# Kernel optimization log

Measured on AMD Instinct MI355X. Metric: run time of the kernel, lower is better.

## Reference

```python
import jax, jax.numpy as jnp
import numpy as np

B, L, D = 2, 384, 128
N, DHS, DHP = 8, 16, 4  # heads, scalar head dim, point head dim
D_SCALAR = N * DHS          # 128
D_POINT = N * DHP * 3       # 96
D_OUT_IN = D_SCALAR + D * N + D_POINT + N * DHP  # 1280


def setup_inputs() -> dict:
    key = jax.random.key(0)
    ks = jax.random.split(key, 14)
    sc = 0.05
    x = jax.random.normal(ks[0], (B, L, D), dtype=jnp.float32)
    e = jax.random.normal(ks[1], (B, L, L, D), dtype=jnp.float32)
    r = jax.random.normal(ks[2], (B, L, 3, 3), dtype=jnp.float32)
    t = jax.random.normal(ks[3], (B, L, 3), dtype=jnp.float32)
    Wq_s = jax.random.normal(ks[4], (D, D_SCALAR)) * sc
    Wk_s = jax.random.normal(ks[5], (D, D_SCALAR)) * sc
    Wv_s = jax.random.normal(ks[6], (D, D_SCALAR)) * sc
    Wb = jax.random.normal(ks[7], (D, N)) * sc
    Wq_p = jax.random.normal(ks[8], (D, D_POINT)) * sc
    Wk_p = jax.random.normal(ks[9], (D, D_POINT)) * sc
    Wv_p = jax.random.normal(ks[10], (D, D_POINT)) * sc
    gamma = jnp.full((N,), float(np.log(np.exp(1.0) - 1.0)), dtype=jnp.float32)
    Wo = jax.random.normal(ks[11], (D_OUT_IN, D)) * sc
    bo = jnp.zeros((D,), dtype=jnp.float32)
    return {"x": x, "e": e, "r": r, "t": t, "Wq_s": Wq_s, "Wk_s": Wk_s,
            "Wv_s": Wv_s, "Wb": Wb, "Wq_p": Wq_p, "Wk_p": Wk_p,
            "Wv_p": Wv_p, "gamma": gamma, "Wo": Wo, "bo": bo}


def _heads_scalar(y):  # (b,l,n*d) -> (b,n,l,d)
    b, l, _ = y.shape
    return y.reshape(b, l, N, DHS).transpose(0, 2, 1, 3)


def _heads_point(y):  # (b,l,n*p*3) -> (b,n,l,p,3)
    b, l, _ = y.shape
    return y.reshape(b, l, N, DHP, 3).transpose(0, 2, 1, 3, 4)


def reference(x, e, r, t, Wq_s, Wk_s, Wv_s, Wb, Wq_p, Wk_p, Wv_p, gamma, Wo, bo):
    b, l, _ = x.shape
    qs = _heads_scalar(x @ Wq_s)
    ks_ = _heads_scalar(x @ Wk_s)
    vs = _heads_scalar(x @ Wv_s)

    # local points -> global frame: x_row @ r + t (note row-vector convention)
    t_b = t[:, None, :, None, :]  # (b,1,l,1,3)
    qp = jnp.einsum('bnlpk,blkc->bnlpc', _heads_point(x @ Wq_p), r) + t_b
    kp = jnp.einsum('bnlpk,blkc->bnlpc', _heads_point(x @ Wk_p), r) + t_b
    vp = jnp.einsum('bnlpk,blkc->bnlpc', _heads_point(x @ Wv_p), r) + t_b

    logit_scalar = jnp.einsum('bnid,bnjd->bnij', qs, ks_) * (DHS ** -0.5)
    bias_pair = jnp.einsum('bijd,dn->bnij', e, Wb)

    # sum_{p,c} (q_i - k_j)^2 via norm expansion (same math, no O(l^2 p 3) tensor)
    qq = jnp.sum(qp * qp, axis=(-1, -2))  # (b,n,i)
    kk = jnp.sum(kp * kp, axis=(-1, -2))  # (b,n,j)
    cross = jnp.einsum('bnipc,bnjpc->bnij', qp, kp)
    dist2 = qq[..., :, None] + kk[..., None, :] - 2.0 * cross
    logit_point = (-0.5 * 0.25) * gamma[None, :, None, None] * dist2

    logit = (3.0 ** -0.5) * (logit_scalar + bias_pair + logit_point)
    attn = jax.nn.softmax(logit, axis=-1)  # (b,n,i,j)

    out_scalar = jnp.einsum('bnij,bnjd->bnid', attn, vs)
    out_scalar = out_scalar.transpose(0, 2, 1, 3).reshape(b, l, N * DHS)

    out_pair = jnp.einsum('bnij,bijd->bnid', attn, e)
    out_pair = out_pair.transpose(0, 2, 1, 3).reshape(b, l, N * D)

    op = jnp.einsum('bnij,bnjpc->bnipc', attn, vp)
    # inverse transform: (x - t) @ r^T  -> out[c] = sum_k (x-t)[k] * r[c,k]
    op_local = jnp.einsum('bnipk,bick->bnipc', op - t_b, r)
    op_norm = jnp.linalg.norm(op_local, axis=-1)  # (b,n,i,p)

    out_point = op_local.transpose(0, 2, 1, 3, 4).reshape(b, l, N * DHP * 3)
    out_norm = op_norm.transpose(0, 2, 1, 3).reshape(b, l, N * DHP)

    out = jnp.concatenate([out_scalar, out_pair, out_point, out_norm], axis=-1)
    return out @ Wo + bo
```

## Files before the change

### kernel.cpp

```cpp
#include <hip/hip_runtime.h>
#include <hip/hip_bf16.h>

#define BB 2
#define LL 384
#define DD 128
#define NH 8

typedef const float* fp32p;

__global__ __launch_bounds__(128) void k_proj(
    fp32p x, fp32p r, fp32p tvec,
    fp32p Wqs, fp32p Wks, fp32p Wvs,
    fp32p Wqp, fp32p Wkp, fp32p Wvp,
    float* qs, float* ks, float* vs,
    float* qp, float* kp, float* vp)
{
  int bl = blockIdx.x;
  int t = threadIdx.x;
  __shared__ float xs[128];
  __shared__ float yq[96], yk[96], yv[96];
  xs[t] = x[bl*128 + t];
  __syncthreads();
  float aq = 0.f, ak = 0.f, av = 0.f;
  for (int d = 0; d < 128; ++d) {
    float xv = xs[d];
    aq += xv * Wqs[d*128 + t];
    ak += xv * Wks[d*128 + t];
    av += xv * Wvs[d*128 + t];
  }
  int b = bl / LL, l = bl - (bl / LL) * LL;
  int n = t >> 4, dhs = t & 15;
  int rowbase = (b*NH + n)*LL + l;
  qs[rowbase*16 + dhs] = aq;
  ks[rowbase*16 + dhs] = ak;
  vs[rowbase*16 + dhs] = av;
  if (t < 96) {
    float pq = 0.f, pk = 0.f, pv = 0.f;
    for (int d = 0; d < 128; ++d) {
      float xv = xs[d];
      pq += xv * Wqp[d*96 + t];
      pk += xv * Wkp[d*96 + t];
      pv += xv * Wvp[d*96 + t];
    }
    yq[t] = pq; yk[t] = pk; yv[t] = pv;
  }
  __syncthreads();
  if (t < 96) {
    int np = t / 12;
    int rem = t - np*12;
    int p = rem / 3, c = rem - p*3;
    float rr0 = r[(bl*3 + 0)*3 + c];
    float rr1 = r[(bl*3 + 1)*3 + c];
    float rr2 = r[(bl*3 + 2)*3 + c];
    float tt  = tvec[bl*3 + c];
    int base = np*12 + p*3;
    int prow = (b*NH + np)*LL + l;
    qp[prow*12 + p*3 + c] = yq[base]*rr0 + yq[base+1]*rr1 + yq[base+2]*rr2 + tt;
    kp[prow*12 + p*3 + c] = yk[base]*rr0 + yk[base+1]*rr1 + yk[base+2]*rr2 + tt;
    vp[prow*12 + p*3 + c] = yv[base]*rr0 + yv[base+1]*rr1 + yv[base+2]*rr2 + tt;
  }
}

__global__ __launch_bounds__(256) void k_bias(fp32p e, fp32p Wb, float* bias)
{
  __shared__ float WbS[128*8];
  for (int idx = threadIdx.x; idx < 1024; idx += 256) WbS[idx] = Wb[idx];
  __syncthreads();
  int tid = blockIdx.x*256 + threadIdx.x;
  int b = tid / (LL*LL);
  int rem = tid - b*(LL*LL);
  int i = rem / LL, j = rem - (rem / LL)*LL;
  const float4* erow = reinterpret_cast<const float4*>(e) + (size_t)tid * 32;
  float acc[8] = {0,0,0,0,0,0,0,0};
  for (int it = 0; it < 32; ++it) {
    float4 v4 = erow[it];
    float vv[4] = {v4.x, v4.y, v4.z, v4.w};
    #pragma unroll
    for (int k = 0; k < 4; ++k) {
      float v = vv[k];
      const float* wr = &WbS[(it*4 + k)*8];
      #pragma unroll
      for (int nn = 0; nn < 8; ++nn) acc[nn] += v * wr[nn];
    }
  }
  #pragma unroll
  for (int nn = 0; nn < 8; ++nn)
    bias[(((size_t)(b*NH + nn)*LL + i)*LL) + j] = acc[nn];
}

__global__ __launch_bounds__(256) void k_attn(
    const float* qs, const float* ks, const float* qp, const float* kp,
    fp32p gamma, float* attn)
{
  int row = blockIdx.x*4 + (threadIdx.x >> 6);
  int lane = threadIdx.x & 63;
  int bn = row / LL;
  int n = bn & 7;
  int rowbase = bn * LL;
  float q[16];
  const float4* q4 = reinterpret_cast<const float4*>(qs + (size_t)row*16);
  #pragma unroll
  for (int k2 = 0; k2 < 4; ++k2) { float4 v = q4[k2]; q[4*k2]=v.x; q[4*k2+1]=v.y; q[4*k2+2]=v.z; q[4*k2+3]=v.w; }
  float qpv[12];
  const float4* p4 = reinterpret_cast<const float4*>(qp + (size_t)row*12);
  #pragma unroll
  for (int k2 = 0; k2 < 3; ++k2) { float4 v = p4[k2]; qpv[4*k2]=v.x; qpv[4*k2+1]=v.y; qpv[4*k2+2]=v.z; qpv[4*k2+3]=v.w; }
  float qq = 0.f;
  #pragma unroll
  for (int k2 = 0; k2 < 12; ++k2) qq += qpv[k2]*qpv[k2];
  float coef = -0.125f * gamma[n];
  float lg[6];
  float* arow = attn + (size_t)row*LL;
  #pragma unroll
  for (int jj = 0; jj < 6; ++jj) {
    int j = lane + jj*64;
    const float4* k4 = reinterpret_cast<const float4*>(ks + (size_t)(rowbase + j)*16);
    float dots = 0.f;
    #pragma unroll
    for (int k2 = 0; k2 < 4; ++k2) { float4 v = k4[k2]; dots += q[4*k2]*v.x + q[4*k2+1]*v.y + q[4*k2+2]*v.z + q[4*k2+3]*v.w; }
    const float4* kp4 = reinterpret_cast<const float4*>(kp + (size_t)(rowbase + j)*12);
    float cross = 0.f, kk = 0.f;
    #pragma unroll
    for (int k2 = 0; k2 < 3; ++k2) {
      float4 v = kp4[k2];
      cross += qpv[4*k2]*v.x + qpv[4*k2+1]*v.y + qpv[4*k2+2]*v.z + qpv[4*k2+3]*v.w;
      kk += v.x*v.x + v.y*v.y + v.z*v.z + v.w*v.w;
    }
    float bs = arow[j];
    lg[jj] = 0.57735027f * (0.25f*dots + bs + coef*(qq + kk - 2.f*cross));
  }
  float m = lg[0];
  #pragma unroll
  for (int jj = 1; jj < 6; ++jj) m = fmaxf(m, lg[jj]);
  #pragma unroll
  for (int off = 32; off >= 1; off >>= 1) m = fmaxf(m, __shfl_xor(m, off, 64));
  float el[6]; float s = 0.f;
  #pragma unroll
  for (int jj = 0; jj < 6; ++jj) { el[jj] = __expf(lg[jj] - m); s += el[jj]; }
  #pragma unroll
  for (int off = 32; off >= 1; off >>= 1) s += __shfl_xor(s, off, 64);
  float inv = 1.f / s;
  #pragma unroll
  for (int jj = 0; jj < 6; ++jj) arow[lane + jj*64] = el[jj]*inv;
}

__global__ __launch_bounds__(256) void k_av(
    const float* attn, const float* vs, const float* vp, float* cat, float* opb)
{
  int tid = blockIdx.x*256 + threadIdx.x;
  int row = tid >> 5;
  int dim = tid & 31;
  if (dim >= 28) return;
  int i = row % LL;
  int bn = row / LL;
  int rowbase = bn * LL;
  const float* arow = attn + (size_t)row*LL;
  const float* src; int stride;
  if (dim < 16) { src = vs + (size_t)rowbase*16 + dim; stride = 16; }
  else          { src = vp + (size_t)rowbase*12 + (dim - 16); stride = 12; }
  float acc = 0.f;
  for (int j = 0; j < LL; ++j) acc += arow[j] * src[(size_t)j*stride];
  int b = bn >> 3, n = bn & 7;
  if (dim < 16) cat[((size_t)(b*LL + i))*1280 + n*16 + dim] = acc;
  else          opb[(size_t)row*12 + (dim - 16)] = acc;
}

__global__ __launch_bounds__(256) void k_pair(fp32p e, const float* attn, float* cat)
{
  int bi = blockIdx.x;
  int b = bi / LL, i = bi - (bi / LL)*LL;
  __shared__ float attnS[8*384];
  __shared__ float redS[128*9];
  for (int idx = threadIdx.x; idx < 8*384; idx += 256) {
    int n = idx / 384, j = idx - n*384;
    attnS[idx] = attn[(((size_t)(b*NH + n)*LL + i)*LL) + j];
  }
  __syncthreads();
  int t = threadIdx.x;
  int oct = t & 15;
  int n = (t >> 4) & 7;
  int half = t >> 7;
  const float4* ebase = reinterpret_cast<const float4*>(e) + (size_t)bi*LL*32;
  const float* an = attnS + n*384;
  float acc[8] = {0,0,0,0,0,0,0,0};
  for (int jj = 0; jj < 192; ++jj) {
    int j = 2*jj + half;
    float4 va = ebase[j*32 + oct*2];
    float4 vb = ebase[j*32 + oct*2 + 1];
    float a = an[j];
    acc[0] += a * va.x; acc[1] += a * va.y; acc[2] += a * va.z; acc[3] += a * va.w;
    acc[4] += a * vb.x; acc[5] += a * vb.y; acc[6] += a * vb.z; acc[7] += a * vb.w;
  }
  if (half) {
    #pragma unroll
    for (int k = 0; k < 8; ++k) redS[(t - 128)*9 + k] = acc[k];
  }
  __syncthreads();
  if (!half) {
    float* dst = cat + (size_t)bi*1280 + 128 + n*128 + oct*8;
    #pragma unroll
    for (int k = 0; k < 8; ++k) dst[k] = acc[k] + redS[t*9 + k];
  }
}

__global__ __launch_bounds__(256) void k_pt(const float* opb, fp32p r, fp32p tvec, float* cat)
{
  int tid = blockIdx.x*256 + threadIdx.x;
  int p = tid & 3;
  int row = tid >> 2;
  int i = row % LL;
  int bn = row / LL;
  int b = bn >> 3, n = bn & 7;
  int bi = b*LL + i;
  float o[3];
  #pragma unroll
  for (int k = 0; k < 3; ++k)
    o[k] = opb[(size_t)row*12 + p*3 + k] - tvec[bi*3 + k];
  float loc[3];
  #pragma unroll
  for (int c = 0; c < 3; ++c) {
    float s = 0.f;
    #pragma unroll
    for (int k = 0; k < 3; ++k) s += o[k] * r[(bi*3 + c)*3 + k];
    loc[c] = s;
  }
  float* dst = cat + (size_t)bi*1280;
  dst[1152 + n*12 + p*3 + 0] = loc[0];
  dst[1152 + n*12 + p*3 + 1] = loc[1];
  dst[1152 + n*12 + p*3 + 2] = loc[2];
  dst[1248 + n*4 + p] = sqrtf(loc[0]*loc[0] + loc[1]*loc[1] + loc[2]*loc[2]);
}

__global__ __launch_bounds__(128) void k_out(const float* cat, fp32p Wo, fp32p bo,
                                             float* out)
{
  __shared__ float catS[4*1280];
  int row0 = blockIdx.x*4;
  for (int idx = threadIdx.x; idx < 4*1280; idx += 128)
    catS[idx] = cat[(size_t)row0*1280 + idx];
  __syncthreads();
  int t = threadIdx.x;
  float bov = bo[t];
  float a0 = bov, a1 = bov, a2 = bov, a3 = bov;
  for (int k = 0; k < 1280; ++k) {
    float w = Wo[k*128 + t];
    a0 += catS[k]        * w;
    a1 += catS[1280 + k] * w;
    a2 += catS[2560 + k] * w;
    a3 += catS[3840 + k] * w;
  }
  out[(size_t)(row0 + 0)*128 + t] = a0;
  out[(size_t)(row0 + 1)*128 + t] = a1;
  out[(size_t)(row0 + 2)*128 + t] = a2;
  out[(size_t)(row0 + 3)*128 + t] = a3;
}

extern "C" void kernel_launch(void* const* d_in, const int* in_sizes, int n_in,
                              void* d_out, int out_size, void* d_ws, size_t ws_size,
                              hipStream_t stream)
{
  fp32p x    = (fp32p)d_in[0];
  fp32p e    = (fp32p)d_in[1];
  fp32p r    = (fp32p)d_in[2];
  fp32p tv   = (fp32p)d_in[3];
  fp32p Wqs  = (fp32p)d_in[4];
  fp32p Wks  = (fp32p)d_in[5];
  fp32p Wvs  = (fp32p)d_in[6];
  fp32p Wb   = (fp32p)d_in[7];
  fp32p Wqp  = (fp32p)d_in[8];
  fp32p Wkp  = (fp32p)d_in[9];
  fp32p Wvp  = (fp32p)d_in[10];
  fp32p gam  = (fp32p)d_in[11];
  fp32p Wo   = (fp32p)d_in[12];
  fp32p bo   = (fp32p)d_in[13];
  float* out = (float*)d_out;

  float* qs   = (float*)d_ws;
  float* ks   = qs + 98304;
  float* vs   = ks + 98304;
  float* qp   = vs + 98304;
  float* kp   = qp + 73728;
  float* vp   = kp + 73728;
  float* attn = vp + 73728;
  float* opb  = attn + 2359296;
  float* cat  = opb + 73728;

  k_proj<<<768, 128, 0, stream>>>(x, r, tv, Wqs, Wks, Wvs, Wqp, Wkp, Wvp,
                                  qs, ks, vs, qp, kp, vp);
  k_bias<<<1152, 256, 0, stream>>>(e, Wb, attn);
  k_attn<<<1536, 256, 0, stream>>>(qs, ks, qp, kp, gam, attn);
  k_av<<<768, 256, 0, stream>>>(attn, vs, vp, cat, opb);
  k_pair<<<768, 256, 0, stream>>>(e, attn, cat);
  k_pt<<<96, 256, 0, stream>>>(opb, r, tv, cat);
  k_out<<<192, 128, 0, stream>>>(cat, Wo, bo, out);
}
```

Before: 422.3 us.

## Fuse bias, logits, softmax, AV, pair and point stages into one per-row kernel

```diff
diff --git a/kernel.cpp b/kernel.cpp
--- a/kernel.cpp
+++ b/kernel.cpp
@@ -1,9 +1,6 @@
 #include <hip/hip_runtime.h>
-#include <hip/hip_bf16.h>
-
-#define BB 2
+
 #define LL 384
-#define DD 128
 #define NH 8
 
 typedef const float* fp32p;
@@ -15,244 +12,242 @@
     float* qs, float* ks, float* vs,
     float* qp, float* kp, float* vp)
 {
-  int bl = blockIdx.x;
   int t = threadIdx.x;
-  __shared__ float xs[128];
-  __shared__ float yq[96], yk[96], yv[96];
-  xs[t] = x[bl*128 + t];
-  __syncthreads();
-  float aq = 0.f, ak = 0.f, av = 0.f;
+  int bl0 = blockIdx.x * 4;
+  __shared__ float xs[4][128];
+  __shared__ float yq[4][96], yk[4][96], yv[4][96];
+  #pragma unroll
+  for (int rr = 0; rr < 4; ++rr) xs[rr][t] = x[(bl0 + rr)*128 + t];
+  __syncthreads();
+  float aq[4] = {0,0,0,0}, ak[4] = {0,0,0,0}, av[4] = {0,0,0,0};
+  float pq[4] = {0,0,0,0}, pk[4] = {0,0,0,0}, pv[4] = {0,0,0,0};
+  bool pt_act = (t < 96);
   for (int d = 0; d < 128; ++d) {
-    float xv = xs[d];
-    aq += xv * Wqs[d*128 + t];
-    ak += xv * Wks[d*128 + t];
-    av += xv * Wvs[d*128 + t];
-  }
-  int b = bl / LL, l = bl - (bl / LL) * LL;
+    float wq = Wqs[d*128 + t], wk = Wks[d*128 + t], wv = Wvs[d*128 + t];
+    #pragma unroll
+    for (int rr = 0; rr < 4; ++rr) {
+      float xv = xs[rr][d];
+      aq[rr] += xv*wq; ak[rr] += xv*wk; av[rr] += xv*wv;
+    }
+    if (pt_act) {
+      float uq = Wqp[d*96 + t], uk = Wkp[d*96 + t], uv = Wvp[d*96 + t];
+      #pragma unroll
+      for (int rr = 0; rr < 4; ++rr) {
+        float xv = xs[rr][d];
+        pq[rr] += xv*uq; pk[rr] += xv*uk; pv[rr] += xv*uv;
+      }
+    }
+  }
   int n = t >> 4, dhs = t & 15;
-  int rowbase = (b*NH + n)*LL + l;
-  qs[rowbase*16 + dhs] = aq;
-  ks[rowbase*16 + dhs] = ak;
-  vs[rowbase*16 + dhs] = av;
-  if (t < 96) {
-    float pq = 0.f, pk = 0.f, pv = 0.f;
-    for (int d = 0; d < 128; ++d) {
-      float xv = xs[d];
-      pq += xv * Wqp[d*96 + t];
-      pk += xv * Wkp[d*96 + t];
-      pv += xv * Wvp[d*96 + t];
-    }
-    yq[t] = pq; yk[t] = pk; yv[t] = pv;
-  }
-  __syncthreads();
-  if (t < 96) {
+  #pragma unroll
+  for (int rr = 0; rr < 4; ++rr) {
+    int bl = bl0 + rr;
+    int b = bl / LL, l = bl - (bl / LL)*LL;
+    int rowbase = (b*NH + n)*LL + l;
+    qs[rowbase*16 + dhs] = aq[rr];
+    ks[rowbase*16 + dhs] = ak[rr];
+    vs[rowbase*16 + dhs] = av[rr];
+  }
+  if (pt_act) {
+    #pragma unroll
+    for (int rr = 0; rr < 4; ++rr) { yq[rr][t] = pq[rr]; yk[rr][t] = pk[rr]; yv[rr][t] = pv[rr]; }
+  }
+  __syncthreads();
+  if (pt_act) {
     int np = t / 12;
     int rem = t - np*12;
     int p = rem / 3, c = rem - p*3;
-    float rr0 = r[(bl*3 + 0)*3 + c];
-    float rr1 = r[(bl*3 + 1)*3 + c];
-    float rr2 = r[(bl*3 + 2)*3 + c];
-    float tt  = tvec[bl*3 + c];
     int base = np*12 + p*3;
-    int prow = (b*NH + np)*LL + l;
-    qp[prow*12 + p*3 + c] = yq[base]*rr0 + yq[base+1]*rr1 + yq[base+2]*rr2 + tt;
-    kp[prow*12 + p*3 + c] = yk[base]*rr0 + yk[base+1]*rr1 + yk[base+2]*rr2 + tt;
-    vp[prow*12 + p*3 + c] = yv[base]*rr0 + yv[base+1]*rr1 + yv[base+2]*rr2 + tt;
-  }
-}
-
-__global__ __launch_bounds__(256) void k_bias(fp32p e, fp32p Wb, float* bias)
-{
-  __shared__ float WbS[128*8];
-  for (int idx = threadIdx.x; idx < 1024; idx += 256) WbS[idx] = Wb[idx];
-  __syncthreads();
-  int tid = blockIdx.x*256 + threadIdx.x;
-  int b = tid / (LL*LL);
-  int rem = tid - b*(LL*LL);
-  int i = rem / LL, j = rem - (rem / LL)*LL;
-  const float4* erow = reinterpret_cast<const float4*>(e) + (size_t)tid * 32;
-  float acc[8] = {0,0,0,0,0,0,0,0};
-  for (int it = 0; it < 32; ++it) {
-    float4 v4 = erow[it];
-    float vv[4] = {v4.x, v4.y, v4.z, v4.w};
-    #pragma unroll
-    for (int k = 0; k < 4; ++k) {
-      float v = vv[k];
-      const float* wr = &WbS[(it*4 + k)*8];
-      #pragma unroll
-      for (int nn = 0; nn < 8; ++nn) acc[nn] += v * wr[nn];
-    }
-  }
-  #pragma unroll
-  for (int nn = 0; nn < 8; ++nn)
-    bias[(((size_t)(b*NH + nn)*LL + i)*LL) + j] = acc[nn];
-}
-
-__global__ __launch_bounds__(256) void k_attn(
-    const float* qs, const float* ks, const float* qp, const float* kp,
-    fp32p gamma, float* attn)
-{
-  int row = blockIdx.x*4 + (threadIdx.x >> 6);
-  int lane = threadIdx.x & 63;
-  int bn = row / LL;
-  int n = bn & 7;
-  int rowbase = bn * LL;
-  float q[16];
-  const float4* q4 = reinterpret_cast<const float4*>(qs + (size_t)row*16);
-  #pragma unroll
-  for (int k2 = 0; k2 < 4; ++k2) { float4 v = q4[k2]; q[4*k2]=v.x; q[4*k2+1]=v.y; q[4*k2+2]=v.z; q[4*k2+3]=v.w; }
-  float qpv[12];
-  const float4* p4 = reinterpret_cast<const float4*>(qp + (size_t)row*12);
-  #pragma unroll
-  for (int k2 = 0; k2 < 3; ++k2) { float4 v = p4[k2]; qpv[4*k2]=v.x; qpv[4*k2+1]=v.y; qpv[4*k2+2]=v.z; qpv[4*k2+3]=v.w; }
-  float qq = 0.f;
-  #pragma unroll
-  for (int k2 = 0; k2 < 12; ++k2) qq += qpv[k2]*qpv[k2];
-  float coef = -0.125f * gamma[n];
-  float lg[6];
-  float* arow = attn + (size_t)row*LL;
-  #pragma unroll
-  for (int jj = 0; jj < 6; ++jj) {
-    int j = lane + jj*64;
-    const float4* k4 = reinterpret_cast<const float4*>(ks + (size_t)(rowbase + j)*16);
-    float dots = 0.f;
-    #pragma unroll
-    for (int k2 = 0; k2 < 4; ++k2) { float4 v = k4[k2]; dots += q[4*k2]*v.x + q[4*k2+1]*v.y + q[4*k2+2]*v.z + q[4*k2+3]*v.w; }
-    const float4* kp4 = reinterpret_cast<const float4*>(kp + (size_t)(rowbase + j)*12);
-    float cross = 0.f, kk = 0.f;
-    #pragma unroll
-    for (int k2 = 0; k2 < 3; ++k2) {
-      float4 v = kp4[k2];
-      cross += qpv[4*k2]*v.x + qpv[4*k2+1]*v.y + qpv[4*k2+2]*v.z + qpv[4*k2+3]*v.w;
-      kk += v.x*v.x + v.y*v.y + v.z*v.z + v.w*v.w;
-    }
-    float bs = arow[j];
-    lg[jj] = 0.57735027f * (0.25f*dots + bs + coef*(qq + kk - 2.f*cross));
-  }
-  float m = lg[0];
-  #pragma unroll
-  for (int jj = 1; jj < 6; ++jj) m = fmaxf(m, lg[jj]);
-  #pragma unroll
-  for (int off = 32; off >= 1; off >>= 1) m = fmaxf(m, __shfl_xor(m, off, 64));
-  float el[6]; float s = 0.f;
-  #pragma unroll
-  for (int jj = 0; jj < 6; ++jj) { el[jj] = __expf(lg[jj] - m); s += el[jj]; }
-  #pragma unroll
-  for (int off = 32; off >= 1; off >>= 1) s += __shfl_xor(s, off, 64);
-  float inv = 1.f / s;
-  #pragma unroll
-  for (int jj = 0; jj < 6; ++jj) arow[lane + jj*64] = el[jj]*inv;
-}
-
-__global__ __launch_bounds__(256) void k_av(
-    const float* attn, const float* vs, const float* vp, float* cat, float* opb)
-{
-  int tid = blockIdx.x*256 + threadIdx.x;
-  int row = tid >> 5;
-  int dim = tid & 31;
-  if (dim >= 28) return;
-  int i = row % LL;
-  int bn = row / LL;
-  int rowbase = bn * LL;
-  const float* arow = attn + (size_t)row*LL;
-  const float* src; int stride;
-  if (dim < 16) { src = vs + (size_t)rowbase*16 + dim; stride = 16; }
-  else          { src = vp + (size_t)rowbase*12 + (dim - 16); stride = 12; }
-  float acc = 0.f;
-  for (int j = 0; j < LL; ++j) acc += arow[j] * src[(size_t)j*stride];
-  int b = bn >> 3, n = bn & 7;
-  if (dim < 16) cat[((size_t)(b*LL + i))*1280 + n*16 + dim] = acc;
-  else          opb[(size_t)row*12 + (dim - 16)] = acc;
-}
-
-__global__ __launch_bounds__(256) void k_pair(fp32p e, const float* attn, float* cat)
+    #pragma unroll
+    for (int rr = 0; rr < 4; ++rr) {
+      int bl = bl0 + rr;
+      int b = bl / LL, l = bl - (bl / LL)*LL;
+      float rr0 = r[(bl*3 + 0)*3 + c];
+      float rr1 = r[(bl*3 + 1)*3 + c];
+      float rr2 = r[(bl*3 + 2)*3 + c];
+      float tt  = tvec[bl*3 + c];
+      int prow = (b*NH + np)*LL + l;
+      qp[prow*12 + p*3 + c] = yq[rr][base]*rr0 + yq[rr][base+1]*rr1 + yq[rr][base+2]*rr2 + tt;
+      kp[prow*12 + p*3 + c] = yk[rr][base]*rr0 + yk[rr][base+1]*rr1 + yk[rr][base+2]*rr2 + tt;
+      vp[prow*12 + p*3 + c] = yv[rr][base]*rr0 + yv[rr][base+1]*rr1 + yv[rr][base+2]*rr2 + tt;
+    }
+  }
+}
+
+__global__ __launch_bounds__(256) void k_fused(
+    fp32p e, fp32p Wb, fp32p gamma, fp32p r, fp32p tvec,
+    const float* qs, const float* ks, const float* vs,
+    const float* qp, const float* kp, const float* vp,
+    float* cat)
 {
   int bi = blockIdx.x;
   int b = bi / LL, i = bi - (bi / LL)*LL;
-  __shared__ float attnS[8*384];
+  int t = threadIdx.x;
+  __shared__ float attnS[8*385];
   __shared__ float redS[128*9];
-  for (int idx = threadIdx.x; idx < 8*384; idx += 256) {
-    int n = idx / 384, j = idx - n*384;
-    attnS[idx] = attn[(((size_t)(b*NH + n)*LL + i)*LL) + j];
-  }
-  __syncthreads();
+  __shared__ float opS[96];
+
+  const float* ebase = e + (size_t)bi*LL*128;
+
+  for (int j = t; j < LL; j += 256) {
+    const float4* er = reinterpret_cast<const float4*>(ebase + j*128);
+    float accb[8] = {0,0,0,0,0,0,0,0};
+    for (int it = 0; it < 32; ++it) {
+      float4 v4 = er[it];
+      float vv[4] = {v4.x, v4.y, v4.z, v4.w};
+      #pragma unroll
+      for (int k = 0; k < 4; ++k) {
+        float ev = vv[k];
+        int d = it*4 + k;
+        #pragma unroll
+        for (int nn = 0; nn < 8; ++nn) accb[nn] += ev * Wb[d*8 + nn];
+      }
+    }
+    #pragma unroll
+    for (int nn = 0; nn < 8; ++nn) {
+      int rowq = (b*NH + nn)*LL + i;
+      int rowk = (b*NH + nn)*LL + j;
+      const float4* k4  = reinterpret_cast<const float4*>(ks + (size_t)rowk*16);
+      const float4* q4  = reinterpret_cast<const float4*>(qs + (size_t)rowq*16);
+      float dots = 0.f;
+      #pragma unroll
+      for (int k2 = 0; k2 < 4; ++k2) {
+        float4 kv = k4[k2]; float4 qv = q4[k2];
+        dots += qv.x*kv.x + qv.y*kv.y + qv.z*kv.z + qv.w*kv.w;
+      }
+      const float4* kp4 = reinterpret_cast<const float4*>(kp + (size_t)rowk*12);
+      const float4* qp4 = reinterpret_cast<const float4*>(qp + (size_t)rowq*12);
+      float cross = 0.f, kk = 0.f, qq = 0.f;
+      #pragma unroll
+      for (int k2 = 0; k2 < 3; ++k2) {
+        float4 pv = kp4[k2]; float4 qv = qp4[k2];
+        cross += qv.x*pv.x + qv.y*pv.y + qv.z*pv.z + qv.w*pv.w;
+        kk += pv.x*pv.x + pv.y*pv.y + pv.z*pv.z + pv.w*pv.w;
+        qq += qv.x*qv.x + qv.y*qv.y + qv.z*qv.z + qv.w*qv.w;
+      }
+      float coef = -0.125f * gamma[nn];
+      attnS[nn*385 + j] = 0.57735027f * (0.25f*dots + accb[nn] + coef*(qq + kk - 2.f*cross));
+    }
+  }
+  __syncthreads();
+
+  {
+    int wv = t >> 6, lane = t & 63;
+    #pragma unroll
+    for (int nn2 = 0; nn2 < 2; ++nn2) {
+      int n = wv*2 + nn2;
+      float v[6];
+      #pragma unroll
+      for (int q = 0; q < 6; ++q) v[q] = attnS[n*385 + lane + q*64];
+      float m = v[0];
+      #pragma unroll
+      for (int q = 1; q < 6; ++q) m = fmaxf(m, v[q]);
+      #pragma unroll
+      for (int off = 32; off >= 1; off >>= 1) m = fmaxf(m, __shfl_xor(m, off, 64));
+      float s = 0.f;
+      #pragma unroll
+      for (int q = 0; q < 6; ++q) { v[q] = __expf(v[q] - m); s += v[q]; }
+      #pragma unroll
+      for (int off = 32; off >= 1; off >>= 1) s += __shfl_xor(s, off, 64);
+      float inv = 1.f / s;
+      #pragma unroll
+      for (int q = 0; q < 6; ++q) attnS[n*385 + lane + q*64] = v[q]*inv;
+    }
+  }
+  __syncthreads();
+
+  if (t < 224) {
+    int n = t / 28, d = t - (t / 28)*28;
+    const float* an = attnS + n*385;
+    int rowbase = (b*NH + n)*LL;
+    float acc = 0.f;
+    if (d < 16) {
+      const float* src = vs + (size_t)rowbase*16 + d;
+      for (int j = 0; j < LL; ++j) acc += an[j] * src[j*16];
+      cat[(size_t)bi*1280 + n*16 + d] = acc;
+    } else {
+      const float* src = vp + (size_t)rowbase*12 + (d - 16);
+      for (int j = 0; j < LL; ++j) acc += an[j] * src[j*12];
+      opS[n*12 + (d - 16)] = acc;
+    }
+  }
+  __syncthreads();
+
+  {
+    int oct = t & 15, n3 = (t >> 4) & 7, half = t >> 7;
+    const float* an = attnS + n3*385;
+    const float4* e4 = reinterpret_cast<const float4*>(ebase);
+    float acc[8] = {0,0,0,0,0,0,0,0};
+    for (int jj = 0; jj < 192; ++jj) {
+      int j = 2*jj + half;
+      float4 va = e4[j*32 + oct*2];
+      float4 vb = e4[j*32 + oct*2 + 1];
+      float a = an[j];
+      acc[0] += a*va.x; acc[1] += a*va.y; acc[2] += a*va.z; acc[3] += a*va.w;
+      acc[4] += a*vb.x; acc[5] += a*vb.y; acc[6] += a*vb.z; acc[7] += a*vb.w;
+    }
+    if (half) {
+      #pragma unroll
+      for (int k = 0; k < 8; ++k) redS[(t - 128)*9 + k] = acc[k];
+    }
+    __syncthreads();
+    if (!half) {
+      float* dst = cat + (size_t)bi*1280 + 128 + n3*128 + oct*8;
+      #pragma unroll
+      for (int k = 0; k < 8; ++k) dst[k] = acc[k] + redS[t*9 + k];
+    }
+  }
+
+  if (t < 32) {
+    int n = t >> 2, p = t & 3;
+    float o[3];
+    #pragma unroll
+    for (int k = 0; k < 3; ++k) o[k] = opS[n*12 + p*3 + k] - tvec[bi*3 + k];
+    float loc[3];
+    #pragma unroll
+    for (int c = 0; c < 3; ++c) {
+      float s = 0.f;
+      #pragma unroll
+      for (int k = 0; k < 3; ++k) s += o[k] * r[(bi*3 + c)*3 + k];
+      loc[c] = s;
+    }
+    float* dst = cat + (size_t)bi*1280;
+    dst[1152 + n*12 + p*3 + 0] = loc[0];
+    dst[1152 + n*12 + p*3 + 1] = loc[1];
+    dst[1152 + n*12 + p*3 + 2] = loc[2];
+    dst[1248 + n*4 + p] = sqrtf(loc[0]*loc[0] + loc[1]*loc[1] + loc[2]*loc[2]);
+  }
+}
+
+__global__ __launch_bounds__(256) void k_out(const float* cat, fp32p Wo, fp32p bo,
+                                             float* out)
+{
+  int r0 = blockIdx.x*4;
   int t = threadIdx.x;
-  int oct = t & 15;
-  int n = (t >> 4) & 7;
-  int half = t >> 7;
-  const float4* ebase = reinterpret_cast<const float4*>(e) + (size_t)bi*LL*32;
-  const float* an = attnS + n*384;
-  float acc[8] = {0,0,0,0,0,0,0,0};
-  for (int jj = 0; jj < 192; ++jj) {
-    int j = 2*jj + half;
-    float4 va = ebase[j*32 + oct*2];
-    float4 vb = ebase[j*32 + oct*2 + 1];
-    float a = an[j];
-    acc[0] += a * va.x; acc[1] += a * va.y; acc[2] += a * va.z; acc[3] += a * va.w;
-    acc[4] += a * vb.x; acc[5] += a * vb.y; acc[6] += a * vb.z; acc[7] += a * vb.w;
-  }
-  if (half) {
-    #pragma unroll
-    for (int k = 0; k < 8; ++k) redS[(t - 128)*9 + k] = acc[k];
-  }
-  __syncthreads();
-  if (!half) {
-    float* dst = cat + (size_t)bi*1280 + 128 + n*128 + oct*8;
-    #pragma unroll
-    for (int k = 0; k < 8; ++k) dst[k] = acc[k] + redS[t*9 + k];
-  }
-}
-
-__global__ __launch_bounds__(256) void k_pt(const float* opb, fp32p r, fp32p tvec, float* cat)
-{
-  int tid = blockIdx.x*256 + threadIdx.x;
-  int p = tid & 3;
-  int row = tid >> 2;
-  int i = row % LL;
-  int bn = row / LL;
-  int b = bn >> 3, n = bn & 7;
-  int bi = b*LL + i;
-  float o[3];
-  #pragma unroll
-  for (int k = 0; k < 3; ++k)
-    o[k] = opb[(size_t)row*12 + p*3 + k] - tvec[bi*3 + k];
-  float loc[3];
-  #pragma unroll
-  for (int c = 0; c < 3; ++c) {
-    float s = 0.f;
-    #pragma unroll
-    for (int k = 0; k < 3; ++k) s += o[k] * r[(bi*3 + c)*3 + k];
-    loc[c] = s;
-  }
-  float* dst = cat + (size_t)bi*1280;
-  dst[1152 + n*12 + p*3 + 0] = loc[0];
-  dst[1152 + n*12 + p*3 + 1] = loc[1];
-  dst[1152 + n*12 + p*3 + 2] = loc[2];
-  dst[1248 + n*4 + p] = sqrtf(loc[0]*loc[0] + loc[1]*loc[1] + loc[2]*loc[2]);
-}
-
-__global__ __launch_bounds__(128) void k_out(const float* cat, fp32p Wo, fp32p bo,
-                                             float* out)
-{
   __shared__ float catS[4*1280];
-  int row0 = blockIdx.x*4;
-  for (int idx = threadIdx.x; idx < 4*1280; idx += 128)
-    catS[idx] = cat[(size_t)row0*1280 + idx];
-  __syncthreads();
-  int t = threadIdx.x;
-  float bov = bo[t];
-  float a0 = bov, a1 = bov, a2 = bov, a3 = bov;
-  for (int k = 0; k < 1280; ++k) {
-    float w = Wo[k*128 + t];
+  __shared__ float redO[4*128];
+  for (int idx = t; idx < 4*1280; idx += 256)
+    catS[idx] = cat[(size_t)r0*1280 + idx];
+  __syncthreads();
+  int c = t & 127, half = t >> 7;
+  int k0 = half*640;
+  float a0 = 0.f, a1 = 0.f, a2 = 0.f, a3 = 0.f;
+  for (int k = k0; k < k0 + 640; ++k) {
+    float w = Wo[k*128 + c];
     a0 += catS[k]        * w;
     a1 += catS[1280 + k] * w;
     a2 += catS[2560 + k] * w;
     a3 += catS[3840 + k] * w;
   }
-  out[(size_t)(row0 + 0)*128 + t] = a0;
-  out[(size_t)(row0 + 1)*128 + t] = a1;
-  out[(size_t)(row0 + 2)*128 + t] = a2;
-  out[(size_t)(row0 + 3)*128 + t] = a3;
+  if (half) { redO[c] = a0; redO[128 + c] = a1; redO[256 + c] = a2; redO[384 + c] = a3; }
+  __syncthreads();
+  if (!half) {
+    float bv = bo[c];
+    out[(size_t)(r0 + 0)*128 + c] = a0 + redO[c]       + bv;
+    out[(size_t)(r0 + 1)*128 + c] = a1 + redO[128 + c] + bv;
+    out[(size_t)(r0 + 2)*128 + c] = a2 + redO[256 + c] + bv;
+    out[(size_t)(r0 + 3)*128 + c] = a3 + redO[384 + c] + bv;
+  }
 }
 
 extern "C" void kernel_launch(void* const* d_in, const int* in_sizes, int n_in,
@@ -275,22 +270,16 @@
   fp32p bo   = (fp32p)d_in[13];
   float* out = (float*)d_out;
 
-  float* qs   = (float*)d_ws;
-  float* ks   = qs + 98304;
-  float* vs   = ks + 98304;
-  float* qp   = vs + 98304;
-  float* kp   = qp + 73728;
-  float* vp   = kp + 73728;
-  float* attn = vp + 73728;
-  float* opb  = attn + 2359296;
-  float* cat  = opb + 73728;
-
-  k_proj<<<768, 128, 0, stream>>>(x, r, tv, Wqs, Wks, Wvs, Wqp, Wkp, Wvp,
+  float* qs  = (float*)d_ws;
+  float* ks  = qs + 98304;
+  float* vs  = ks + 98304;
+  float* qp  = vs + 98304;
+  float* kp  = qp + 73728;
+  float* vp  = kp + 73728;
+  float* cat = vp + 73728;
+
+  k_proj<<<192, 128, 0, stream>>>(x, r, tv, Wqs, Wks, Wvs, Wqp, Wkp, Wvp,
                                   qs, ks, vs, qp, kp, vp);
-  k_bias<<<1152, 256, 0, stream>>>(e, Wb, attn);
-  k_attn<<<1536, 256, 0, stream>>>(qs, ks, qp, kp, gam, attn);
-  k_av<<<768, 256, 0, stream>>>(attn, vs, vp, cat, opb);
-  k_pair<<<768, 256, 0, stream>>>(e, attn, cat);
-  k_pt<<<96, 256, 0, stream>>>(opb, r, tv, cat);
-  k_out<<<192, 128, 0, stream>>>(cat, Wo, bo, out);
-}
+  k_fused<<<768, 256, 0, stream>>>(e, Wb, gam, r, tv, qs, ks, vs, qp, kp, vp, cat);
+  k_out<<<192, 256, 0, stream>>>(cat, Wo, bo, out);
+}
```

Result: slower. 605.2 us (+43.3%).
